# Kernel tuning notes

Hardware: AMD Instinct MI355X
Metric: run time of the kernel (lower is better)

Reference implementation:

```python
import jax, jax.numpy as jnp
import numpy as np

GROUP_SIZE = 128


def dequant_rtn(qweight, scale, zero_point):
    # qweight: [O, I] int, scale/zero_point: [O, I//GROUP_SIZE]
    O, I = qweight.shape
    G = scale.shape[1]
    gs = I // G
    q = qweight.reshape(O, G, gs).astype(jnp.float32)
    zp = zero_point.astype(jnp.float32)[:, :, None]
    w = (q - zp) * scale[:, :, None]
    return w.reshape(O, I)


def setup_inputs() -> dict:
    key = jax.random.key(0)
    k1, k2, k3, k4, k5 = jax.random.split(key, 5)
    B, S, I, O = 2, 2048, 4096, 11008
    G = I // GROUP_SIZE
    x = jax.random.normal(k1, (B, S, I), dtype=jnp.float32)
    qweight = jax.random.randint(k2, (O, I), 0, 16, dtype=jnp.int32)
    scale = jax.random.uniform(k3, (O, G), dtype=jnp.float32) * 0.02 + 1e-3
    zero_point = jax.random.randint(k4, (O, G), 0, 16, dtype=jnp.int32)
    bias = jax.random.normal(k5, (O,), dtype=jnp.float32)
    return {"x": x, "qweight": qweight, "scale": scale,
            "zero_point": zero_point, "bias": bias}


def reference(x, qweight, scale, zero_point, bias):
    # weight-only path: dequant weight, then F.linear(x, w, bias)
    w = dequant_rtn(qweight, scale, zero_point)  # [O, I] fp32
    return jnp.einsum('bsi,oi->bso', x, w) + bias
```

## Files before the change

kernel.cpp:

```cpp
#include <hip/hip_runtime.h>
#include <cstdint>
#include <cstddef>

typedef __attribute__((ext_vector_type(4))) int i32x4;
typedef __bf16 bf16;
typedef __attribute__((ext_vector_type(8))) __bf16 bf16x8;
typedef __attribute__((ext_vector_type(4))) float f32x4;

#define BM 128
#define BN 128
#define BKB 128
#define GROUP_M 16
#define GM256 4
#define NXCD 8

__device__ __forceinline__ unsigned bf16_rne(float f) {
  unsigned u = __float_as_uint(f);
  unsigned r = 0x7FFFu + ((u >> 16) & 1u);
  return ((u + r) >> 16) & 0xFFFFu;
}
__device__ __forceinline__ unsigned pack2(float a, float b) {
  return bf16_rne(a) | (bf16_rne(b) << 16);
}
__device__ __forceinline__ int pack4i8(int a, int b, int c, int d) {
  return (a & 0xFF) | ((b & 0xFF) << 8) | ((c & 0xFF) << 16) | (d << 24);
}
__device__ __forceinline__ int q_i8(float v) {
  v = fminf(fmaxf(v, -127.0f), 127.0f);
  return __float2int_rn(v);
}

__global__ __launch_bounds__(256) void prep_kernel(
    const float* __restrict__ x, char* __restrict__ xq, float* __restrict__ xscale,
    int M,
    const int* __restrict__ q, const float* __restrict__ scale,
    const int* __restrict__ zp, char* __restrict__ wq, float* __restrict__ wscale,
    int K, int G) {
  __shared__ float red[4];
  const int b = blockIdx.x;
  const int tid = threadIdx.x;

  if (b >= M) {
    const int row = b - M;
    const float* srow = scale + (size_t)row * G;
    const int*   zrow = zp + (size_t)row * G;
    const int lane = tid & 63;
    const int g0 = lane & 31;
    const float s0 = srow[g0];
    const float z0 = (float)zrow[g0];
    float bnd = s0 * fmaxf(z0, 15.0f - z0);
#pragma unroll
    for (int off = 16; off >= 1; off >>= 1)
      bnd = fmaxf(bnd, __shfl_xor(bnd, off));
    const float inv = 127.0f / bnd;
    const int4* src = (const int4*)(q + (size_t)row * K);
    int* dst = (int*)(wq + (size_t)row * K);
#pragma unroll
    for (int i = 0; i < 4; ++i) {
      const int j = tid + 256 * i;
      const int g = j >> 5;
      const float fs = srow[g] * inv;
      const float fo = -(float)zrow[g] * srow[g] * inv;
      int4 qv = src[j];
      dst[j] = pack4i8(__float2int_rn(fmaf((float)qv.x, fs, fo)),
                       __float2int_rn(fmaf((float)qv.y, fs, fo)),
                       __float2int_rn(fmaf((float)qv.z, fs, fo)),
                       __float2int_rn(fmaf((float)qv.w, fs, fo)));
    }
    if (tid == 0) wscale[row] = bnd * (1.0f / 127.0f);
    return;
  }

  float f[16];
  const float4* src = (const float4*)(x + (size_t)b * K);
#pragma unroll
  for (int i = 0; i < 4; ++i) {
    float4 v = src[tid + 256 * i];
    f[4 * i + 0] = v.x; f[4 * i + 1] = v.y;
    f[4 * i + 2] = v.z; f[4 * i + 3] = v.w;
  }

  float m = 0.f;
#pragma unroll
  for (int j = 0; j < 16; ++j) m = fmaxf(m, fabsf(f[j]));
#pragma unroll
  for (int off = 32; off >= 1; off >>= 1) m = fmaxf(m, __shfl_xor(m, off));
  if ((tid & 63) == 0) red[tid >> 6] = m;
  __syncthreads();
  m = fmaxf(fmaxf(red[0], red[1]), fmaxf(red[2], red[3]));

  const float inv = m > 0.f ? 127.0f / m : 0.f;
  int pk[4];
#pragma unroll
  for (int i = 0; i < 4; ++i)
    pk[i] = pack4i8(q_i8(f[4 * i + 0] * inv), q_i8(f[4 * i + 1] * inv),
                    q_i8(f[4 * i + 2] * inv), q_i8(f[4 * i + 3] * inv));

  int* dst_i32 = (int*)(xq + (size_t)b * K);
#pragma unroll
  for (int i = 0; i < 4; ++i) dst_i32[tid + 256 * i] = pk[i];

  if (tid == 0) xscale[b] = m * (1.0f / 127.0f);
}

typedef __attribute__((address_space(1))) void gas_void;
typedef __attribute__((address_space(3))) void las_void;

__device__ __forceinline__ void load_lds16(const void* g, void* l) {
  __builtin_amdgcn_global_load_lds((gas_void*)g, (las_void*)l, 16, 0, 0);
}


#define STAGE_A_H(buf, h, ktb) do {                                           \
    load_lds16(A + abase + (size_t)(ktb) + aoff0 + (size_t)(h) * 64 * K,      \
               &Al[buf][(h) * 8192 + dw]);                                    \
    load_lds16(A + abase + (size_t)(ktb) + aoff1 + (size_t)(h) * 64 * K,      \
               &Al[buf][16384 + (h) * 8192 + dw]);                            \
  } while (0)

#define STAGE_B_H(buf, h, ktb) do {                                           \
    load_lds16(Bw + bbase + (size_t)(ktb) + boff0 + (size_t)(h) * 32 * K,     \
               &Bl[buf][(h) * 16384 + dw]);                                   \
    load_lds16(Bw + bbase + (size_t)(ktb) + boff1 + (size_t)(h) * 32 * K,     \
               &Bl[buf][(h) * 16384 + 8192 + dw]);                            \
  } while (0)

__global__ __launch_bounds__(512) void gemm_i8_256(
    const char* __restrict__ A,
    const char* __restrict__ Bw,
    const float* __restrict__ ascale,
    const float* __restrict__ bscale,
    const float* __restrict__ bias,
    float* __restrict__ C,
    int M, int N, int K) {
  __shared__ __align__(16) char Al[2][256 * 128];
  __shared__ __align__(16) char Bl[2][256 * 128];
  const int tid  = threadIdx.x;
  const int wave = tid >> 6;
  const int lane = tid & 63;
  const int quad = lane >> 4;
  const int l16  = lane & 15;
  const int wq3  = wave & 3;
  const int wmb  = (wave >> 2) * 128;
  const int wnb  = wq3 * 64;

  const int nbm = M / 256, nbn = N / 256;
  const int cpx = (nbm * nbn) / NXCD;
  const int swz = ((int)blockIdx.x % NXCD) * cpx + (int)blockIdx.x / NXCD;
  const int per_group = GM256 * nbn;
  const int gid = swz / per_group;
  const int rem = swz - gid * per_group;
  int gm = nbm - gid * GM256; if (gm > GM256) gm = GM256;
  const int bm = (gid * GM256 + (rem % gm)) * 256;
  const int bn = (rem / gm) * 256;

  const int r0 = tid >> 3;
  const int kq16 = (((tid & 7) ^ (r0 & 7)) * 16);
  const size_t aoff0 = (size_t)r0 * K + kq16;
  const size_t aoff1 = aoff0 + (size_t)128 * K;
  const size_t boff0 = (size_t)((r0 >> 5) * 64 + (r0 & 31)) * K + kq16;
  const size_t boff1 = boff0 + (size_t)128 * K;
  const int dw = wave * 1024;
  const size_t abase = (size_t)bm * K;
  const size_t bbase = (size_t)bn * K;
  const int NT = K / 128;

  i32x4 acc[8][4];
#pragma unroll
  for (int i = 0; i < 8; ++i)
#pragma unroll
    for (int j = 0; j < 4; ++j)
      acc[i][j] = (i32x4){0, 0, 0, 0};

  STAGE_A_H(0, 0, 0);
  STAGE_A_H(0, 1, 0);
  STAGE_B_H(0, 0, 0);
  STAGE_B_H(0, 1, 0);
  asm volatile("s_waitcnt vmcnt(0)" ::: "memory");
  __builtin_amdgcn_s_barrier();
  __builtin_amdgcn_sched_barrier(0);

  for (int t = 0; t < NT; ++t) {
    const int cur = t & 1;
    const int nxt = cur ^ 1;
    const int kt1 = (t + 1) * 128;
    const bool s1 = (t + 1) < NT;

    if (s1) {
      STAGE_A_H(nxt, 0, kt1);
      STAGE_A_H(nxt, 1, kt1);
      STAGE_B_H(nxt, 0, kt1);
      STAGE_B_H(nxt, 1, kt1);
    }
    __builtin_amdgcn_sched_barrier(0);

    i32x4 afr0[8], bfr0[4], afr1[8], bfr1[4];
#pragma unroll
    for (int tm = 0; tm < 8; ++tm) {
      int row = wmb + tm * 16 + l16;
      int kq  = quad;
      afr0[tm] = *(const i32x4*)&Al[cur][(row * 8 + (kq ^ (row & 7))) * 16];
    }
#pragma unroll
    for (int j = 0; j < 4; ++j) {
      int p  = (j >> 1) * 128 + wq3 * 32 + (j & 1) * 16 + l16;
      int kq = quad;
      bfr0[j] = *(const i32x4*)&Bl[cur][(p * 8 + (kq ^ (p & 7))) * 16];
    }
    __builtin_amdgcn_sched_barrier(0);

#pragma unroll
    for (int tm = 0; tm < 8; ++tm) {
      int row = wmb + tm * 16 + l16;
      int kq  = 4 + quad;
      afr1[tm] = *(const i32x4*)&Al[cur][(row * 8 + (kq ^ (row & 7))) * 16];
    }
#pragma unroll
    for (int j = 0; j < 4; ++j) {
      int p  = (j >> 1) * 128 + wq3 * 32 + (j & 1) * 16 + l16;
      int kq = 4 + quad;
      bfr1[j] = *(const i32x4*)&Bl[cur][(p * 8 + (kq ^ (p & 7))) * 16];
    }
    __builtin_amdgcn_sched_barrier(0);

    __builtin_amdgcn_s_setprio(1);
#pragma unroll
    for (int tm = 0; tm < 8; ++tm)
#pragma unroll
      for (int j = 0; j < 4; ++j)
        acc[tm][j] = __builtin_amdgcn_mfma_i32_16x16x64_i8(
            afr0[tm], bfr0[j], acc[tm][j], 0, 0, 0);
    __builtin_amdgcn_s_setprio(0);
    __builtin_amdgcn_sched_barrier(0);

    __builtin_amdgcn_s_setprio(1);
#pragma unroll
    for (int tm = 0; tm < 8; ++tm)
#pragma unroll
      for (int j = 0; j < 4; ++j)
        acc[tm][j] = __builtin_amdgcn_mfma_i32_16x16x64_i8(
            afr1[tm], bfr1[j], acc[tm][j], 0, 0, 0);
    __builtin_amdgcn_s_setprio(0);

    asm volatile("s_waitcnt vmcnt(0)" ::: "memory");
    __builtin_amdgcn_s_barrier();
    __builtin_amdgcn_sched_barrier(0);
  }

#pragma unroll
  for (int tn = 0; tn < 4; ++tn) {
    int col = bn + wnb + tn * 16 + l16;
    float bv = bias[col];
    float ws = bscale[col];
#pragma unroll
    for (int tm = 0; tm < 8; ++tm) {
      int row0 = bm + wmb + tm * 16 + quad * 4;
#pragma unroll
      for (int v = 0; v < 4; ++v) {
        float val = ascale[row0 + v] * ws * (float)acc[tm][tn][v] + bv;
        __builtin_nontemporal_store(val, &C[(size_t)(row0 + v) * N + col]);
      }
    }
  }
}

__global__ __launch_bounds__(256) void gemm_i8_kernel(
    const char* __restrict__ A, const char* __restrict__ Bw,
    const float* __restrict__ ascale, const float* __restrict__ bscale,
    const float* __restrict__ bias, float* __restrict__ C,
    int M, int N, int K) {
  __shared__ __align__(16) char Alds[BM * BKB];
  __shared__ __align__(16) char Blds[BN * BKB];
  const int tid  = threadIdx.x;
  const int wave = tid >> 6;
  const int lane = tid & 63;
  const int quad = lane >> 4;
  const int l16  = lane & 15;

  const int nbm = M / BM;
  const int nbn = N / BN;
  int flat = blockIdx.x;
  int per_group = GROUP_M * nbn;
  int gid = flat / per_group;
  int rem = flat - gid * per_group;
  int gm = nbm - gid * GROUP_M;
  if (gm > GROUP_M) gm = GROUP_M;
  const int bm = (gid * GROUP_M + (rem % gm)) * BM;
  const int bn = (rem / gm) * BN;

  const int wm = (wave & 1) * 64;
  const int wn = (wave >> 1) * 64;

  i32x4 acc[4][4];
#pragma unroll
  for (int i = 0; i < 4; ++i)
#pragma unroll
    for (int j = 0; j < 4; ++j)
      acc[i][j] = (i32x4){0, 0, 0, 0};

  for (int kt = 0; kt < K; kt += BKB) {
#pragma unroll
    for (int t = 0; t < 4; ++t) {
      int s0 = (wave * 4 + t) * 64;
      int s  = s0 + lane;
      int m  = s >> 3;
      int kq = (s & 7) ^ (m & 7);
      load_lds16(A  + (size_t)(bm + m) * K + kt + kq * 16, &Alds[s0 * 16]);
      load_lds16(Bw + (size_t)(bn + m) * K + kt + kq * 16, &Blds[s0 * 16]);
    }
    __syncthreads();

#pragma unroll
    for (int ks = 0; ks < 2; ++ks) {
      i32x4 af[4], bfr[4];
#pragma unroll
      for (int tm = 0; tm < 4; ++tm) {
        int m  = wm + tm * 16 + l16;
        int kq = ks * 4 + quad;
        af[tm] = *(const i32x4*)&Alds[(m * 8 + (kq ^ (m & 7))) * 16];
      }
#pragma unroll
      for (int tn = 0; tn < 4; ++tn) {
        int n  = wn + tn * 16 + l16;
        int kq = ks * 4 + quad;
        bfr[tn] = *(const i32x4*)&Blds[(n * 8 + (kq ^ (n & 7))) * 16];
      }
#pragma unroll
      for (int tm = 0; tm < 4; ++tm)
#pragma unroll
        for (int tn = 0; tn < 4; ++tn)
          acc[tm][tn] = __builtin_amdgcn_mfma_i32_16x16x64_i8(
              af[tm], bfr[tn], acc[tm][tn], 0, 0, 0);
    }
    __syncthreads();
  }

#pragma unroll
  for (int tn = 0; tn < 4; ++tn) {
    int col = bn + wn + tn * 16 + l16;
    float bv = bias[col];
    float ws = bscale[col];
#pragma unroll
    for (int tm = 0; tm < 4; ++tm) {
      int row0 = bm + wm + tm * 16 + quad * 4;
#pragma unroll
      for (int v = 0; v < 4; ++v) {
        float val = ascale[row0 + v] * ws * (float)acc[tm][tn][v] + bv;
        __builtin_nontemporal_store(val, &C[(size_t)(row0 + v) * N + col]);
      }
    }
  }
}

__global__ __launch_bounds__(256) void gemm_fused_kernel(
    const float* __restrict__ X, const int* __restrict__ Q,
    const float* __restrict__ scale, const int* __restrict__ zp,
    const float* __restrict__ bias, float* __restrict__ C,
    int M, int N, int K, int G) {
  __shared__ __align__(16) bf16 Alds[128 * 64];
  __shared__ __align__(16) bf16 Blds[128 * 64];
  const int tid  = threadIdx.x;
  const int wave = tid >> 6;
  const int lane = tid & 63;
  const int quad = lane >> 4;
  const int l16  = lane & 15;
  const int bm = blockIdx.y * 128;
  const int bn = blockIdx.x * 128;
  const int wm = (wave & 1) * 64;
  const int wn = (wave >> 1) * 64;

  f32x4 acc[4][4];
#pragma unroll
  for (int i = 0; i < 4; ++i)
#pragma unroll
    for (int j = 0; j < 4; ++j)
      acc[i][j] = (f32x4){0.f, 0.f, 0.f, 0.f};

  for (int kt = 0; kt < K; kt += 64) {
#pragma unroll
    for (int i = 0; i < 4; ++i) {
      int c = tid + i * 256;
      int m = c >> 3;
      int kq = (c & 7) ^ (m & 7);
      const float* src = X + (size_t)(bm + m) * K + kt + kq * 8;
      float4 v0 = *(const float4*)src;
      float4 v1 = *(const float4*)(src + 4);
      uint4 p;
      p.x = pack2(v0.x, v0.y); p.y = pack2(v0.z, v0.w);
      p.z = pack2(v1.x, v1.y); p.w = pack2(v1.z, v1.w);
      *(uint4*)&Alds[c * 8] = p;
    }
#pragma unroll
    for (int i = 0; i < 4; ++i) {
      int c = tid + i * 256;
      int n = c >> 3;
      int kq = (c & 7) ^ (n & 7);
      int kcol = kt + kq * 8;
      size_t row = (size_t)(bn + n);
      int g = kcol >> 7;
      float s = scale[row * G + g];
      float z = (float)zp[row * G + g];
      const int* src = Q + row * K + kcol;
      int4 q0 = *(const int4*)src;
      int4 q1 = *(const int4*)(src + 4);
      uint4 p;
      p.x = pack2(((float)q0.x - z) * s, ((float)q0.y - z) * s);
      p.y = pack2(((float)q0.z - z) * s, ((float)q0.w - z) * s);
      p.z = pack2(((float)q1.x - z) * s, ((float)q1.y - z) * s);
      p.w = pack2(((float)q1.z - z) * s, ((float)q1.w - z) * s);
      *(uint4*)&Blds[c * 8] = p;
    }
    __syncthreads();

#pragma unroll
    for (int ks = 0; ks < 2; ++ks) {
      bf16x8 af[4], bfr[4];
#pragma unroll
      for (int tm = 0; tm < 4; ++tm) {
        int m  = wm + tm * 16 + l16;
        int kq = ks * 4 + quad;
        af[tm] = *(const bf16x8*)&Alds[(m * 8 + (kq ^ (m & 7))) * 8];
      }
#pragma unroll
      for (int tn = 0; tn < 4; ++tn) {
        int n  = wn + tn * 16 + l16;
        int kq = ks * 4 + quad;
        bfr[tn] = *(const bf16x8*)&Blds[(n * 8 + (kq ^ (n & 7))) * 8];
      }
#pragma unroll
      for (int tm = 0; tm < 4; ++tm)
#pragma unroll
        for (int tn = 0; tn < 4; ++tn)
          acc[tm][tn] = __builtin_amdgcn_mfma_f32_16x16x32_bf16(
              af[tm], bfr[tn], acc[tm][tn], 0, 0, 0);
    }
    __syncthreads();
  }

#pragma unroll
  for (int tn = 0; tn < 4; ++tn) {
    int col = bn + wn + tn * 16 + l16;
    float bv = bias[col];
#pragma unroll
    for (int tm = 0; tm < 4; ++tm) {
      int row0 = bm + wm + tm * 16 + quad * 4;
#pragma unroll
      for (int v = 0; v < 4; ++v)
        C[(size_t)(row0 + v) * N + col] = acc[tm][tn][v] + bv;
    }
  }
}

extern "C" void kernel_launch(void* const* d_in, const int* in_sizes, int n_in,
                              void* d_out, int out_size, void* d_ws, size_t ws_size,
                              hipStream_t stream) {
  const float* x     = (const float*)d_in[0];
  const int*   qw    = (const int*)d_in[1];
  const float* scale = (const float*)d_in[2];
  const int*   zp    = (const int*)d_in[3];
  const float* bias  = (const float*)d_in[4];
  float* out = (float*)d_out;

  const int O = in_sizes[4];
  const int I = (int)(in_sizes[1] / O);
  const int M = (int)(in_sizes[0] / I);
  const int G = in_sizes[2] / O;
  const int K = I, N = O;

  size_t off_xq = 0;
  size_t off_xs = off_xq + (size_t)M * K;
  size_t off_wq = (off_xs + (size_t)M * 4 + 255) & ~(size_t)255;
  size_t off_ws_ = off_wq + (size_t)N * K;
  size_t need   = ((off_ws_ + (size_t)N * 4 + 255) & ~(size_t)255);

  if (ws_size >= need && K == 4096) {
    char*  xq = (char*)d_ws + off_xq;
    float* xs = (float*)((char*)d_ws + off_xs);
    char*  wq = (char*)d_ws + off_wq;
    float* wsc = (float*)((char*)d_ws + off_ws_);

    prep_kernel<<<M + N, 256, 0, stream>>>(x, xq, xs, M, qw, scale, zp, wq, wsc, K, G);

    const int nb256 = (M / 256) * (N / 256);
    if ((M % 256) == 0 && (N % 256) == 0 && (nb256 % NXCD) == 0) {
      gemm_i8_256<<<nb256, 512, 0, stream>>>(xq, wq, xs, wsc, bias, out, M, N, K);
    } else {
      int nblocks = (M / BM) * (N / BN);
      gemm_i8_kernel<<<nblocks, 256, 0, stream>>>(xq, wq, xs, wsc, bias, out, M, N, K);
    }
  } else {
    dim3 gemm_grid((unsigned)(N / 128), (unsigned)(M / 128));
    gemm_fused_kernel<<<gemm_grid, 256, 0, stream>>>(x, qw, scale, zp, bias, out,
                                                     M, N, K, G);
  }
}
```

Baseline: 558.0 us.

## Shrink int8 GEMM tile to 256x128 with 64-deep K steps for occupancy

Reworks the large-tile int8 GEMM to use 256x128 output tiles and a K step of 64 instead of 256x256 tiles with K step 128. LDS staging shrinks to 48KB per block with a new 4-chunk XOR swizzle, the accumulator halves, and launch bounds request multiple blocks per CU. The aim is higher occupancy and better tail balance with twice as many blocks. The cost is lower data reuse per loaded byte and twice as many barrier-synchronised k iterations.

```diff
diff --git a/kernel.cpp b/kernel.cpp
--- a/kernel.cpp
+++ b/kernel.cpp
@@ -111,21 +111,16 @@
 }
 
 
-#define STAGE_A_H(buf, h, ktb) do {                                           \
-    load_lds16(A + abase + (size_t)(ktb) + aoff0 + (size_t)(h) * 64 * K,      \
-               &Al[buf][(h) * 8192 + dw]);                                    \
-    load_lds16(A + abase + (size_t)(ktb) + aoff1 + (size_t)(h) * 64 * K,      \
-               &Al[buf][16384 + (h) * 8192 + dw]);                            \
+#define STAGE_A2(buf, ktb) do {                                               \
+    load_lds16(A + abase + (size_t)(ktb) + aoff0, &Al[buf][tid * 16]);        \
+    load_lds16(A + abase + (size_t)(ktb) + aoff1, &Al[buf][(512 + tid) * 16]);\
   } while (0)
 
-#define STAGE_B_H(buf, h, ktb) do {                                           \
-    load_lds16(Bw + bbase + (size_t)(ktb) + boff0 + (size_t)(h) * 32 * K,     \
-               &Bl[buf][(h) * 16384 + dw]);                                   \
-    load_lds16(Bw + bbase + (size_t)(ktb) + boff1 + (size_t)(h) * 32 * K,     \
-               &Bl[buf][(h) * 16384 + 8192 + dw]);                            \
+#define STAGE_B2(buf, ktb) do {                                               \
+    load_lds16(Bw + bbase + (size_t)(ktb) + boff0, &Bl[buf][tid * 16]);       \
   } while (0)
 
-__global__ __launch_bounds__(512) void gemm_i8_256(
+__global__ __launch_bounds__(512, 4) void gemm_i8_256(
     const char* __restrict__ A,
     const char* __restrict__ Bw,
     const float* __restrict__ ascale,
@@ -133,8 +128,8 @@
     const float* __restrict__ bias,
     float* __restrict__ C,
     int M, int N, int K) {
-  __shared__ __align__(16) char Al[2][256 * 128];
-  __shared__ __align__(16) char Bl[2][256 * 128];
+  __shared__ __align__(16) char Al[2][256 * 64];
+  __shared__ __align__(16) char Bl[2][128 * 64];
   const int tid  = threadIdx.x;
   const int wave = tid >> 6;
   const int lane = tid & 63;
@@ -142,9 +137,9 @@
   const int l16  = lane & 15;
   const int wq3  = wave & 3;
   const int wmb  = (wave >> 2) * 128;
-  const int wnb  = wq3 * 64;
-
-  const int nbm = M / 256, nbn = N / 256;
+  const int wnb  = wq3 * 32;
+
+  const int nbm = M / 256, nbn = N / 128;
   const int cpx = (nbm * nbn) / NXCD;
   const int swz = ((int)blockIdx.x % NXCD) * cpx + (int)blockIdx.x / NXCD;
   const int per_group = GM256 * nbn;
@@ -152,30 +147,26 @@
   const int rem = swz - gid * per_group;
   int gm = nbm - gid * GM256; if (gm > GM256) gm = GM256;
   const int bm = (gid * GM256 + (rem % gm)) * 256;
-  const int bn = (rem / gm) * 256;
-
-  const int r0 = tid >> 3;
-  const int kq16 = (((tid & 7) ^ (r0 & 7)) * 16);
-  const size_t aoff0 = (size_t)r0 * K + kq16;
+  const int bn = (rem / gm) * 128;
+
+  const int r0 = tid >> 2;
+  const int kqg = ((tid & 3) ^ ((r0 >> 1) & 3)) * 16;
+  const size_t aoff0 = (size_t)r0 * K + kqg;
   const size_t aoff1 = aoff0 + (size_t)128 * K;
-  const size_t boff0 = (size_t)((r0 >> 5) * 64 + (r0 & 31)) * K + kq16;
-  const size_t boff1 = boff0 + (size_t)128 * K;
-  const int dw = wave * 1024;
+  const size_t boff0 = aoff0;
   const size_t abase = (size_t)bm * K;
   const size_t bbase = (size_t)bn * K;
-  const int NT = K / 128;
-
-  i32x4 acc[8][4];
+  const int NT = K / 64;
+
+  i32x4 acc[8][2];
 #pragma unroll
   for (int i = 0; i < 8; ++i)
 #pragma unroll
-    for (int j = 0; j < 4; ++j)
+    for (int j = 0; j < 2; ++j)
       acc[i][j] = (i32x4){0, 0, 0, 0};
 
-  STAGE_A_H(0, 0, 0);
-  STAGE_A_H(0, 1, 0);
-  STAGE_B_H(0, 0, 0);
-  STAGE_B_H(0, 1, 0);
+  STAGE_A2(0, 0);
+  STAGE_B2(0, 0);
   asm volatile("s_waitcnt vmcnt(0)" ::: "memory");
   __builtin_amdgcn_s_barrier();
   __builtin_amdgcn_sched_barrier(0);
@@ -183,63 +174,30 @@
   for (int t = 0; t < NT; ++t) {
     const int cur = t & 1;
     const int nxt = cur ^ 1;
-    const int kt1 = (t + 1) * 128;
-    const bool s1 = (t + 1) < NT;
-
-    if (s1) {
-      STAGE_A_H(nxt, 0, kt1);
-      STAGE_A_H(nxt, 1, kt1);
-      STAGE_B_H(nxt, 0, kt1);
-      STAGE_B_H(nxt, 1, kt1);
-    }
-    __builtin_amdgcn_sched_barrier(0);
-
-    i32x4 afr0[8], bfr0[4], afr1[8], bfr1[4];
+    const int kt1 = (t + 1) * 64;
+
+    if (t + 1 < NT) {
+      STAGE_A2(nxt, kt1);
+      STAGE_B2(nxt, kt1);
+    }
+
+    i32x4 bfr[2];
+#pragma unroll
+    for (int j = 0; j < 2; ++j) {
+      int n = wnb + j * 16 + l16;
+      bfr[j] = *(const i32x4*)&Bl[cur][(n * 4 + (quad ^ ((n >> 1) & 3))) * 16];
+    }
+    __builtin_amdgcn_s_setprio(1);
 #pragma unroll
     for (int tm = 0; tm < 8; ++tm) {
       int row = wmb + tm * 16 + l16;
-      int kq  = quad;
-      afr0[tm] = *(const i32x4*)&Al[cur][(row * 8 + (kq ^ (row & 7))) * 16];
-    }
-#pragma unroll
-    for (int j = 0; j < 4; ++j) {
-      int p  = (j >> 1) * 128 + wq3 * 32 + (j & 1) * 16 + l16;
-      int kq = quad;
-      bfr0[j] = *(const i32x4*)&Bl[cur][(p * 8 + (kq ^ (p & 7))) * 16];
-    }
-    __builtin_amdgcn_sched_barrier(0);
-
-#pragma unroll
-    for (int tm = 0; tm < 8; ++tm) {
-      int row = wmb + tm * 16 + l16;
-      int kq  = 4 + quad;
-      afr1[tm] = *(const i32x4*)&Al[cur][(row * 8 + (kq ^ (row & 7))) * 16];
-    }
-#pragma unroll
-    for (int j = 0; j < 4; ++j) {
-      int p  = (j >> 1) * 128 + wq3 * 32 + (j & 1) * 16 + l16;
-      int kq = 4 + quad;
-      bfr1[j] = *(const i32x4*)&Bl[cur][(p * 8 + (kq ^ (p & 7))) * 16];
-    }
-    __builtin_amdgcn_sched_barrier(0);
-
-    __builtin_amdgcn_s_setprio(1);
-#pragma unroll
-    for (int tm = 0; tm < 8; ++tm)
-#pragma unroll
-      for (int j = 0; j < 4; ++j)
+      i32x4 afr =
+          *(const i32x4*)&Al[cur][(row * 4 + (quad ^ ((row >> 1) & 3))) * 16];
+#pragma unroll
+      for (int j = 0; j < 2; ++j)
         acc[tm][j] = __builtin_amdgcn_mfma_i32_16x16x64_i8(
-            afr0[tm], bfr0[j], acc[tm][j], 0, 0, 0);
-    __builtin_amdgcn_s_setprio(0);
-    __builtin_amdgcn_sched_barrier(0);
-
-    __builtin_amdgcn_s_setprio(1);
-#pragma unroll
-    for (int tm = 0; tm < 8; ++tm)
-#pragma unroll
-      for (int j = 0; j < 4; ++j)
-        acc[tm][j] = __builtin_amdgcn_mfma_i32_16x16x64_i8(
-            afr1[tm], bfr1[j], acc[tm][j], 0, 0, 0);
+            afr, bfr[j], acc[tm][j], 0, 0, 0);
+    }
     __builtin_amdgcn_s_setprio(0);
 
     asm volatile("s_waitcnt vmcnt(0)" ::: "memory");
@@ -248,7 +206,7 @@
   }
 
 #pragma unroll
-  for (int tn = 0; tn < 4; ++tn) {
+  for (int tn = 0; tn < 2; ++tn) {
     int col = bn + wnb + tn * 16 + l16;
     float bv = bias[col];
     float ws = bscale[col];
@@ -481,9 +439,9 @@
 
     prep_kernel<<<M + N, 256, 0, stream>>>(x, xq, xs, M, qw, scale, zp, wq, wsc, K, G);
 
-    const int nb256 = (M / 256) * (N / 256);
-    if ((M % 256) == 0 && (N % 256) == 0 && (nb256 % NXCD) == 0) {
-      gemm_i8_256<<<nb256, 512, 0, stream>>>(xq, wq, xs, wsc, bias, out, M, N, K);
+    const int nb = (M / 256) * (N / 128);
+    if ((M % 256) == 0 && (N % 128) == 0 && (nb % NXCD) == 0 && (K % 64) == 0) {
+      gemm_i8_256<<<nb, 512, 0, stream>>>(xq, wq, xs, wsc, bias, out, M, N, K);
     } else {
       int nblocks = (M / BM) * (N / BN);
       gemm_i8_kernel<<<nblocks, 256, 0, stream>>>(xq, wq, xs, wsc, bias, out, M, N, K);
```

After: 572.4 us. 2.6% more time.
